# Kernel tuning notes

Hardware: AMD Instinct MI355X
Metric: run time of the kernel (lower is better)

The kernel has to match this reference:

```python
import jax, jax.numpy as jnp
import numpy as np

NUM_HEADS = 8
OUT_DIM = 32


def setup_inputs() -> dict:
    key = jax.random.key(0)
    ks = jax.random.split(key, 9)
    N, E, IN = 50000, 800000, 256
    HD = NUM_HEADS * OUT_DIM
    s = 1.0 / np.sqrt(IN)
    return {
        "h": jax.random.normal(ks[0], (N, IN), jnp.float32),
        "Wq": jax.random.normal(ks[1], (HD, IN), jnp.float32) * s,
        "bq": jax.random.normal(ks[2], (HD,), jnp.float32) * 0.01,
        "Wk": jax.random.normal(ks[3], (HD, IN), jnp.float32) * s,
        "bk": jax.random.normal(ks[4], (HD,), jnp.float32) * 0.01,
        "Wv": jax.random.normal(ks[5], (HD, IN), jnp.float32) * s,
        "bv": jax.random.normal(ks[6], (HD,), jnp.float32) * 0.01,
        "src": jax.random.randint(ks[7], (E,), 0, N, jnp.int32),
        "dst": jax.random.randint(ks[8], (E,), 0, N, jnp.int32),
    }


def reference(h, Wq, bq, Wk, bk, Wv, bv, src, dst):
    N = h.shape[0]
    H, D = NUM_HEADS, OUT_DIM
    # node projections -> [N, H, D]
    Q = (h @ Wq.T + bq).reshape(N, H, D)
    K = (h @ Wk.T + bk).reshape(N, H, D)
    V = (h @ Wv.T + bv).reshape(N, H, D)
    scale = jnp.asarray(np.sqrt(D), h.dtype)
    # per-edge scores: dot(K[src], Q[dst]) over D -> [E, H]
    score = jnp.exp(jnp.clip((K[src] * Q[dst]).sum(-1) / scale, -5.0, 5.0))
    # segment-softmax denominator over destination nodes -> [N, H]
    z = jax.ops.segment_sum(score, dst, num_segments=N)
    alpha = score / z[dst]  # [E, H]; every edge's dst has z > 0
    # weighted aggregation: sum over in-edges of alpha * V[src] -> [N, H, D]
    wV = jax.ops.segment_sum(V[src] * alpha[:, :, None], dst, num_segments=N)
    return wV
```

## Files before the change

kernel.cpp:

```cpp
#include <hip/hip_runtime.h>
#include <hip/hip_bf16.h>


typedef __attribute__((ext_vector_type(8))) short short8;
typedef __attribute__((ext_vector_type(8))) unsigned short ushortx8;
typedef __attribute__((ext_vector_type(4))) unsigned short ushortx4;
typedef __attribute__((ext_vector_type(4))) float floatx4;
typedef __attribute__((ext_vector_type(4))) int intx4;

__device__ __forceinline__ void g2l16(const void* g, void* l) {
    __builtin_amdgcn_global_load_lds(
        (const __attribute__((address_space(1))) unsigned int*)g,
        (__attribute__((address_space(3))) unsigned int*)l, 16, 0, 0);
}

__device__ __forceinline__ float bf2f(unsigned short u) {
    union { unsigned int i; float f; } c; c.i = ((unsigned int)u) << 16; return c.f;
}
__device__ __forceinline__ unsigned short f2bf(float f) {
    __hip_bfloat16 b = __float2bfloat16(f);
    return *reinterpret_cast<unsigned short*>(&b);
}

__device__ __forceinline__ ushortx4 cvt4(floatx4 f) {
    ushortx4 u;
    u.x = f2bf(f.x); u.y = f2bf(f.y); u.z = f2bf(f.z); u.w = f2bf(f.w);
    return u;
}

#define PREP_BH 1563
#define PREP_BW 16
#define PREP_BD 256

__global__ __launch_bounds__(256) void prep(
    const float* __restrict__ h, unsigned short* __restrict__ hb,
    const float* __restrict__ Wq, const float* __restrict__ Wk, const float* __restrict__ Wv,
    unsigned short* __restrict__ Wb,
    const int* __restrict__ dst, int* __restrict__ deg,
    int n4h, int n4w, int E)
{
    const int bid = blockIdx.x;
    const int tid = threadIdx.x;
    if (bid < PREP_BH) {
        const int stride = PREP_BH * 256;
        const floatx4* hs = (const floatx4*)h;
        ushortx4* hd = (ushortx4*)hb;
        int i = bid * 256 + tid;
        for (; i + 3 * stride < n4h; i += 4 * stride) {
            floatx4 f0 = __builtin_nontemporal_load(hs + i);
            floatx4 f1 = __builtin_nontemporal_load(hs + i + stride);
            floatx4 f2 = __builtin_nontemporal_load(hs + i + 2 * stride);
            floatx4 f3 = __builtin_nontemporal_load(hs + i + 3 * stride);
            hd[i] = cvt4(f0);
            hd[i + stride] = cvt4(f1);
            hd[i + 2 * stride] = cvt4(f2);
            hd[i + 3 * stride] = cvt4(f3);
        }
        for (; i < n4h; i += stride) {
            floatx4 f = __builtin_nontemporal_load(hs + i);
            hd[i] = cvt4(f);
        }
    } else if (bid < PREP_BH + 3 * PREP_BW) {
        int b2 = bid - PREP_BH;
        int mat = b2 / PREP_BW;
        const floatx4* ws = (const floatx4*)((mat == 0) ? Wq : (mat == 1) ? Wk : Wv);
        ushortx4* wd = (ushortx4*)(Wb + (size_t)mat * 65536);
        const int stride = PREP_BW * 256;
        int i = (b2 % PREP_BW) * 256 + tid;
        for (; i + 3 * stride < n4w; i += 4 * stride) {
            floatx4 f0 = __builtin_nontemporal_load(ws + i);
            floatx4 f1 = __builtin_nontemporal_load(ws + i + stride);
            floatx4 f2 = __builtin_nontemporal_load(ws + i + 2 * stride);
            floatx4 f3 = __builtin_nontemporal_load(ws + i + 3 * stride);
            wd[i] = cvt4(f0);
            wd[i + stride] = cvt4(f1);
            wd[i + 2 * stride] = cvt4(f2);
            wd[i + 3 * stride] = cvt4(f3);
        }
        for (; i < n4w; i += stride) {
            floatx4 f = __builtin_nontemporal_load(ws + i);
            wd[i] = cvt4(f);
        }
    } else {
        int b3 = bid - PREP_BH - 3 * PREP_BW;
        const int stride = PREP_BD * 256;
        const int ne4 = E >> 2;
        const intx4* ds = (const intx4*)dst;
        int i = b3 * 256 + tid;
        for (; i + stride < ne4; i += 2 * stride) {
            intx4 d0 = __builtin_nontemporal_load(ds + i);
            intx4 d1 = __builtin_nontemporal_load(ds + i + stride);
            atomicAdd(&deg[d0.x], 1); atomicAdd(&deg[d0.y], 1);
            atomicAdd(&deg[d0.z], 1); atomicAdd(&deg[d0.w], 1);
            atomicAdd(&deg[d1.x], 1); atomicAdd(&deg[d1.y], 1);
            atomicAdd(&deg[d1.z], 1); atomicAdd(&deg[d1.w], 1);
        }
        for (; i < ne4; i += stride) {
            intx4 d = __builtin_nontemporal_load(ds + i);
            atomicAdd(&deg[d.x], 1); atomicAdd(&deg[d.y], 1);
            atomicAdd(&deg[d.z], 1); atomicAdd(&deg[d.w], 1);
        }
        if (b3 == 0 && tid == 0) {
            for (int e = ne4 * 4; e < E; e++) atomicAdd(&deg[dst[e]], 1);
        }
    }
}

__global__ __launch_bounds__(256) void qkv_gemm_mfma(
    const unsigned short* __restrict__ hb, const unsigned short* __restrict__ Wb,
    const float* __restrict__ bq, const float* __restrict__ bk, const float* __restrict__ bv,
    unsigned short* __restrict__ Qb, unsigned short* __restrict__ KV, int N)
{
    __shared__ unsigned short Ast[2][128 * 32];
    __shared__ unsigned short Bst[2][128 * 32];

    const int tid = threadIdx.x;
    const int wave = tid >> 6;
    const int lane = tid & 63;
    const int m = lane & 15;
    const int q = lane >> 4;
    const int wr = wave >> 1, wc = wave & 1;

    const int nwg = gridDim.x;
    const int orig = blockIdx.x;
    const int q8 = nwg >> 3, r8 = nwg & 7;
    const int xcd = orig & 7;
    const int wgid = (xcd < r8 ? xcd * (q8 + 1) : r8 * (q8 + 1) + (xcd - r8) * q8)
                     + (orig >> 3);
    const int bx = wgid / 6;
    const int by = wgid % 6;

    const int mbase = bx * 128;
    const int mat = by >> 1;
    const int colbase = (by & 1) * 128;
    const int wrow0 = by * 128;

    const float* bias = (mat == 0) ? bq : (mat == 1) ? bk : bv;

    floatx4 acc[4][4] = {};

    for (int kk = 0; kk < 256; kk += 64) {
#pragma unroll
        for (int c = 0; c < 2; c++) {
#pragma unroll
            for (int t = 0; t < 2; t++) {
                int f = t * 256 + tid;
                int row = f >> 2, kc = f & 3;
                int grow = mbase + row; if (grow > N - 1) grow = N - 1;
                g2l16(hb + (size_t)grow * 256 + kk + c * 32 + kc * 8,
                      Ast[c] + (size_t)(t * 256 + wave * 64) * 8);
            }
#pragma unroll
            for (int t = 0; t < 2; t++) {
                int f = t * 256 + tid;
                int row = f >> 2, kc = f & 3;
                g2l16(Wb + (size_t)(wrow0 + row) * 256 + kk + c * 32 + kc * 8,
                      Bst[c] + (size_t)(t * 256 + wave * 64) * 8);
            }
        }
        __syncthreads();

#pragma unroll
        for (int c = 0; c < 2; c++) {
            short8 a[4], b[4];
#pragma unroll
            for (int i = 0; i < 4; i++) {
                int r = wr * 64 + i * 16 + m;
                a[i] = *(const short8*)&Ast[c][r * 32 + q * 8];
            }
#pragma unroll
            for (int j = 0; j < 4; j++) {
                int cc = wc * 64 + j * 16 + m;
                b[j] = *(const short8*)&Bst[c][cc * 32 + q * 8];
            }
#pragma unroll
            for (int i = 0; i < 4; i++)
#pragma unroll
                for (int j = 0; j < 4; j++)
                    acc[i][j] = __builtin_amdgcn_mfma_f32_16x16x32_bf16(a[i], b[j], acc[i][j], 0, 0, 0);
        }
        __syncthreads();
    }

    float bvj[4];
#pragma unroll
    for (int j = 0; j < 4; j++) bvj[j] = bias[colbase + wc * 64 + j * 16 + m];

    const int col0 = colbase + wc * 64 + m;
#pragma unroll
    for (int i = 0; i < 4; i++) {
#pragma unroll
        for (int r = 0; r < 4; r++) {
            int grow = mbase + wr * 64 + i * 16 + q * 4 + r;
            if (grow < N) {
                if (mat == 0) {
                    unsigned short* op = Qb + (size_t)grow * 256 + col0;
#pragma unroll
                    for (int j = 0; j < 4; j++)
                        __builtin_nontemporal_store(f2bf(acc[i][j][r] + bvj[j]), op + j * 16);
                } else {
                    unsigned short* op = KV + (size_t)grow * 512 + ((mat == 2) ? 256 : 0) + col0;
#pragma unroll
                    for (int j = 0; j < 4; j++)
                        op[j * 16] = f2bf(acc[i][j][r] + bvj[j]);
                }
            }
        }
    }
}

#define SCAN_CHUNK 2048

__global__ void scan_phase1(const int* __restrict__ deg, int* __restrict__ partials, int N) {
    __shared__ int sdata[256];
    int base = blockIdx.x * SCAN_CHUNK;
    int sum = 0;
#pragma unroll
    for (int i = 0; i < 8; i++) {
        int idx = base + threadIdx.x + i * 256;
        if (idx < N) sum += deg[idx];
    }
    sdata[threadIdx.x] = sum;
    __syncthreads();
    for (int s = 128; s > 0; s >>= 1) {
        if (threadIdx.x < (unsigned)s) sdata[threadIdx.x] += sdata[threadIdx.x + s];
        __syncthreads();
    }
    if (threadIdx.x == 0) partials[blockIdx.x] = sdata[0];
}

__global__ void scan_phase2(int* __restrict__ partials, int nb) {
    if (threadIdx.x == 0 && blockIdx.x == 0) {
        int run = 0;
        for (int i = 0; i < nb; i++) { int v = partials[i]; partials[i] = run; run += v; }
    }
}

__global__ void scan_phase3(const int* __restrict__ deg, const int* __restrict__ partials,
                            int* __restrict__ offsets, int* __restrict__ cursor, int N, int E) {
    __shared__ int sdata[256];
    int base = blockIdx.x * SCAN_CHUNK;
    int vals[8];
    int sum = 0;
#pragma unroll
    for (int i = 0; i < 8; i++) {
        int idx = base + threadIdx.x * 8 + i;
        vals[i] = (idx < N) ? deg[idx] : 0;
        sum += vals[i];
    }
    sdata[threadIdx.x] = sum;
    __syncthreads();
    for (int s = 1; s < 256; s <<= 1) {
        int v = sdata[threadIdx.x];
        int add = (threadIdx.x >= (unsigned)s) ? sdata[threadIdx.x - s] : 0;
        __syncthreads();
        sdata[threadIdx.x] = v + add;
        __syncthreads();
    }
    int excl = (threadIdx.x == 0) ? 0 : sdata[threadIdx.x - 1];
    int run = partials[blockIdx.x] + excl;
#pragma unroll
    for (int i = 0; i < 8; i++) {
        int idx = base + threadIdx.x * 8 + i;
        if (idx < N) { offsets[idx] = run; cursor[idx] = run; }
        run += vals[i];
    }
    if (blockIdx.x == 0 && threadIdx.x == 0) offsets[N] = E;
}

__global__ void scatter_edges(const int* __restrict__ dst, const int* __restrict__ src,
                              int* __restrict__ cursor, unsigned short* __restrict__ ssorted,
                              int E) {
    int e4 = (blockIdx.x * 256 + threadIdx.x) * 4;
    if (e4 + 3 < E) {
        intx4 d = __builtin_nontemporal_load((const intx4*)(dst + e4));
        intx4 s = __builtin_nontemporal_load((const intx4*)(src + e4));
        ssorted[atomicAdd(&cursor[d.x], 1)] = (unsigned short)s.x;
        ssorted[atomicAdd(&cursor[d.y], 1)] = (unsigned short)s.y;
        ssorted[atomicAdd(&cursor[d.z], 1)] = (unsigned short)s.z;
        ssorted[atomicAdd(&cursor[d.w], 1)] = (unsigned short)s.w;
    } else {
        for (int e = e4; e < E; e++)
            ssorted[atomicAdd(&cursor[dst[e]], 1)] = (unsigned short)src[e];
    }
}

__global__ __launch_bounds__(256) void edge_agg(
    const unsigned short* __restrict__ Qb, const unsigned short* __restrict__ KV,
    const int* __restrict__ offsets, const unsigned short* __restrict__ ssorted,
    float* __restrict__ out, int N)
{
    const int wave = threadIdx.x >> 6;
    const int lane = threadIdx.x & 63;
    const int half = lane >> 5;
    const int hl = lane & 31;
    const int n = blockIdx.x * 4 + wave;
    if (n >= N) return;

    float q[8];
    {
        ushortx8 qu = __builtin_nontemporal_load((const ushortx8*)(Qb + (size_t)n * 256 + hl * 8));
#pragma unroll
        for (int j = 0; j < 8; j++) q[j] = bf2f(qu[j]);
    }

    float acc[8] = {};
    float z = 0.f;
    const int beg = offsets[n], end = offsets[n + 1];
    const int len = end - beg;
    const int mid = beg + ((len + 1) >> 1);
    const float scale = 0.17677669529663687f;

    int i = half ? mid : beg;
    const int i1 = half ? end : mid;

    for (; i + 1 < i1; i += 2) {
        int s0 = __builtin_nontemporal_load(ssorted + i);
        int s1 = __builtin_nontemporal_load(ssorted + i + 1);
        const unsigned short* p0 = KV + (size_t)s0 * 512 + hl * 8;
        const unsigned short* p1 = KV + (size_t)s1 * 512 + hl * 8;
        ushortx8 k0 = *(const ushortx8*)p0;        ushortx8 v0 = *(const ushortx8*)(p0 + 256);
        ushortx8 k1 = *(const ushortx8*)p1;        ushortx8 v1 = *(const ushortx8*)(p1 + 256);

        float d0 = 0.f, d1 = 0.f;
#pragma unroll
        for (int j = 0; j < 8; j++) {
            d0 = fmaf(bf2f(k0[j]), q[j], d0);
            d1 = fmaf(bf2f(k1[j]), q[j], d1);
        }
        d0 += __shfl_xor(d0, 1); d0 += __shfl_xor(d0, 2);
        d1 += __shfl_xor(d1, 1); d1 += __shfl_xor(d1, 2);
        float e0 = __expf(fminf(5.f, fmaxf(-5.f, d0 * scale)));
        float e1 = __expf(fminf(5.f, fmaxf(-5.f, d1 * scale)));
        z += e0 + e1;
#pragma unroll
        for (int j = 0; j < 8; j++) {
            acc[j] = fmaf(e0, bf2f(v0[j]), acc[j]);
            acc[j] = fmaf(e1, bf2f(v1[j]), acc[j]);
        }
    }
    for (; i < i1; i++) {
        int s = __builtin_nontemporal_load(ssorted + i);
        const unsigned short* p = KV + (size_t)s * 512 + hl * 8;
        ushortx8 k8 = *(const ushortx8*)p;
        ushortx8 v8 = *(const ushortx8*)(p + 256);
        float d = 0.f;
#pragma unroll
        for (int j = 0; j < 8; j++) d = fmaf(bf2f(k8[j]), q[j], d);
        d += __shfl_xor(d, 1); d += __shfl_xor(d, 2);
        float sc = __expf(fminf(5.f, fmaxf(-5.f, d * scale)));
        z += sc;
#pragma unroll
        for (int j = 0; j < 8; j++) acc[j] = fmaf(sc, bf2f(v8[j]), acc[j]);
    }

    z += __shfl_xor(z, 32);
#pragma unroll
    for (int j = 0; j < 8; j++) acc[j] += __shfl_xor(acc[j], 32);

    if (half == 0) {
        float inv = (z > 0.f) ? 1.f / z : 0.f;
        floatx4 o0, o1;
        o0[0] = acc[0] * inv; o0[1] = acc[1] * inv; o0[2] = acc[2] * inv; o0[3] = acc[3] * inv;
        o1[0] = acc[4] * inv; o1[1] = acc[5] * inv; o1[2] = acc[6] * inv; o1[3] = acc[7] * inv;
        floatx4* op = (floatx4*)(out + (size_t)n * 256 + hl * 8);
        __builtin_nontemporal_store(o0, op);
        __builtin_nontemporal_store(o1, op + 1);
    }
}

extern "C" void kernel_launch(void* const* d_in, const int* in_sizes, int n_in,
                              void* d_out, int out_size, void* d_ws, size_t ws_size,
                              hipStream_t stream) {
    const float* h  = (const float*)d_in[0];
    const float* Wq = (const float*)d_in[1];
    const float* bq = (const float*)d_in[2];
    const float* Wk = (const float*)d_in[3];
    const float* bk = (const float*)d_in[4];
    const float* Wv = (const float*)d_in[5];
    const float* bv = (const float*)d_in[6];
    const int*   src = (const int*)d_in[7];
    const int*   dst = (const int*)d_in[8];
    float* out = (float*)d_out;

    const int N = in_sizes[0] / 256;
    const int E = in_sizes[7];

    size_t off = 0;
    auto alloc = [&](size_t bytes) {
        void* p = (char*)d_ws + off;
        off += (bytes + 255) & ~(size_t)255;
        return p;
    };
    unsigned short* Qb = (unsigned short*)alloc((size_t)N * 256 * 2);
    unsigned short* KV = (unsigned short*)alloc((size_t)N * 512 * 2);
    unsigned short* hb = (unsigned short*)alloc((size_t)N * 256 * 2);
    unsigned short* Wb = (unsigned short*)alloc((size_t)768 * 256 * 2);
    int* deg      = (int*)alloc((size_t)N * 4);
    int* offsets  = (int*)alloc((size_t)(N + 1) * 4);
    int* cursor   = (int*)alloc((size_t)N * 4);
    int* partials = (int*)alloc(1024 * 4);
    unsigned short* ssorted = (unsigned short*)alloc((size_t)E * 2);

    hipMemsetAsync(deg, 0, (size_t)N * 4, stream);
    int n4h = (N * 256) / 4;
    int n4w = (256 * 256) / 4;
    prep<<<PREP_BH + 3 * PREP_BW + PREP_BD, 256, 0, stream>>>(
        h, hb, Wq, Wk, Wv, Wb, dst, deg, n4h, n4w, E);

    int nb6 = ((N + 127) / 128) * 6;
    qkv_gemm_mfma<<<nb6, 256, 0, stream>>>(hb, Wb, bq, bk, bv, Qb, KV, N);

    int nscan = (N + SCAN_CHUNK - 1) / SCAN_CHUNK;
    scan_phase1<<<nscan, 256, 0, stream>>>(deg, partials, N);
    scan_phase2<<<1, 64, 0, stream>>>(partials, nscan);
    scan_phase3<<<nscan, 256, 0, stream>>>(deg, partials, offsets, cursor, N, E);
    int bc = (E + 1023) / 1024;
    scatter_edges<<<bc, 256, 0, stream>>>(dst, src, cursor, ssorted, E);

    int ablocks = (N + 3) / 4;
    edge_agg<<<ablocks, 256, 0, stream>>>(Qb, KV, offsets, ssorted, out, N);
}
```

Before: 351.6 us.

## Fold scan block-offset pass into phase3, grid-stride scatter, split aggregation launches

Removes the single-thread scan_phase2 kernel: each scan_phase3 block now sums the preceding block partials itself with a wave shuffle reduction. The edge scatter becomes a fixed 256-block grid-stride loop that processes two int4 chunks per iteration. The h-to-bf16 conversion loop is unrolled from 4 to 8 loads. The edge aggregation kernel is split into four launches over node ranges. The scan change drops a serial launch, but the partial-sum trick assumes at most 64 scan blocks, and the extra aggregation launches add launch overhead.

```diff
diff --git a/kernel.cpp b/kernel.cpp
--- a/kernel.cpp
+++ b/kernel.cpp
@@ -46,15 +46,23 @@
         const floatx4* hs = (const floatx4*)h;
         ushortx4* hd = (ushortx4*)hb;
         int i = bid * 256 + tid;
-        for (; i + 3 * stride < n4h; i += 4 * stride) {
+        for (; i + 7 * stride < n4h; i += 8 * stride) {
             floatx4 f0 = __builtin_nontemporal_load(hs + i);
             floatx4 f1 = __builtin_nontemporal_load(hs + i + stride);
             floatx4 f2 = __builtin_nontemporal_load(hs + i + 2 * stride);
             floatx4 f3 = __builtin_nontemporal_load(hs + i + 3 * stride);
+            floatx4 f4 = __builtin_nontemporal_load(hs + i + 4 * stride);
+            floatx4 f5 = __builtin_nontemporal_load(hs + i + 5 * stride);
+            floatx4 f6 = __builtin_nontemporal_load(hs + i + 6 * stride);
+            floatx4 f7 = __builtin_nontemporal_load(hs + i + 7 * stride);
             hd[i] = cvt4(f0);
             hd[i + stride] = cvt4(f1);
             hd[i + 2 * stride] = cvt4(f2);
             hd[i + 3 * stride] = cvt4(f3);
+            hd[i + 4 * stride] = cvt4(f4);
+            hd[i + 5 * stride] = cvt4(f5);
+            hd[i + 6 * stride] = cvt4(f6);
+            hd[i + 7 * stride] = cvt4(f7);
         }
         for (; i < n4h; i += stride) {
             floatx4 f = __builtin_nontemporal_load(hs + i);
@@ -229,16 +237,18 @@
     if (threadIdx.x == 0) partials[blockIdx.x] = sdata[0];
 }
 
-__global__ void scan_phase2(int* __restrict__ partials, int nb) {
-    if (threadIdx.x == 0 && blockIdx.x == 0) {
-        int run = 0;
-        for (int i = 0; i < nb; i++) { int v = partials[i]; partials[i] = run; run += v; }
-    }
-}
-
 __global__ void scan_phase3(const int* __restrict__ deg, const int* __restrict__ partials,
-                            int* __restrict__ offsets, int* __restrict__ cursor, int N, int E) {
+                            int* __restrict__ offsets, int* __restrict__ cursor,
+                            int N, int E, int nb) {
     __shared__ int sdata[256];
+    __shared__ int sbase;
+    if (threadIdx.x < 64) {
+        int v = ((int)threadIdx.x < nb && (int)threadIdx.x < (int)blockIdx.x)
+                    ? partials[threadIdx.x] : 0;
+#pragma unroll
+        for (int s = 1; s < 64; s <<= 1) v += __shfl_xor(v, s);
+        if (threadIdx.x == 0) sbase = v;
+    }
     int base = blockIdx.x * SCAN_CHUNK;
     int vals[8];
     int sum = 0;
@@ -258,7 +268,7 @@
         __syncthreads();
     }
     int excl = (threadIdx.x == 0) ? 0 : sdata[threadIdx.x - 1];
-    int run = partials[blockIdx.x] + excl;
+    int run = sbase + excl;
 #pragma unroll
     for (int i = 0; i < 8; i++) {
         int idx = base + threadIdx.x * 8 + i;
@@ -268,19 +278,41 @@
     if (blockIdx.x == 0 && threadIdx.x == 0) offsets[N] = E;
 }
 
-__global__ void scatter_edges(const int* __restrict__ dst, const int* __restrict__ src,
-                              int* __restrict__ cursor, unsigned short* __restrict__ ssorted,
-                              int E) {
-    int e4 = (blockIdx.x * 256 + threadIdx.x) * 4;
-    if (e4 + 3 < E) {
-        intx4 d = __builtin_nontemporal_load((const intx4*)(dst + e4));
-        intx4 s = __builtin_nontemporal_load((const intx4*)(src + e4));
+#define SCAT_BLOCKS 256
+__global__ __launch_bounds__(256) void scatter_edges(
+    const int* __restrict__ dst, const int* __restrict__ src,
+    int* __restrict__ cursor, unsigned short* __restrict__ ssorted, int E)
+{
+    const int t = blockIdx.x * 256 + threadIdx.x;
+    const int nt = SCAT_BLOCKS * 256;
+    const int ne4 = E >> 2;
+    const intx4* d4 = (const intx4*)dst;
+    const intx4* s4 = (const intx4*)src;
+    int i = t;
+    for (; i + nt < ne4; i += 2 * nt) {
+        intx4 d0 = __builtin_nontemporal_load(d4 + i);
+        intx4 s0 = __builtin_nontemporal_load(s4 + i);
+        intx4 d1 = __builtin_nontemporal_load(d4 + i + nt);
+        intx4 s1 = __builtin_nontemporal_load(s4 + i + nt);
+        ssorted[atomicAdd(&cursor[d0.x], 1)] = (unsigned short)s0.x;
+        ssorted[atomicAdd(&cursor[d0.y], 1)] = (unsigned short)s0.y;
+        ssorted[atomicAdd(&cursor[d0.z], 1)] = (unsigned short)s0.z;
+        ssorted[atomicAdd(&cursor[d0.w], 1)] = (unsigned short)s0.w;
+        ssorted[atomicAdd(&cursor[d1.x], 1)] = (unsigned short)s1.x;
+        ssorted[atomicAdd(&cursor[d1.y], 1)] = (unsigned short)s1.y;
+        ssorted[atomicAdd(&cursor[d1.z], 1)] = (unsigned short)s1.z;
+        ssorted[atomicAdd(&cursor[d1.w], 1)] = (unsigned short)s1.w;
+    }
+    for (; i < ne4; i += nt) {
+        intx4 d = __builtin_nontemporal_load(d4 + i);
+        intx4 s = __builtin_nontemporal_load(s4 + i);
         ssorted[atomicAdd(&cursor[d.x], 1)] = (unsigned short)s.x;
         ssorted[atomicAdd(&cursor[d.y], 1)] = (unsigned short)s.y;
         ssorted[atomicAdd(&cursor[d.z], 1)] = (unsigned short)s.z;
         ssorted[atomicAdd(&cursor[d.w], 1)] = (unsigned short)s.w;
-    } else {
-        for (int e = e4; e < E; e++)
+    }
+    if (t == 0) {
+        for (int e = ne4 * 4; e < E; e++)
             ssorted[atomicAdd(&cursor[dst[e]], 1)] = (unsigned short)src[e];
     }
 }
@@ -288,14 +320,14 @@
 __global__ __launch_bounds__(256) void edge_agg(
     const unsigned short* __restrict__ Qb, const unsigned short* __restrict__ KV,
     const int* __restrict__ offsets, const unsigned short* __restrict__ ssorted,
-    float* __restrict__ out, int N)
+    float* __restrict__ out, int n0, int n1)
 {
     const int wave = threadIdx.x >> 6;
     const int lane = threadIdx.x & 63;
     const int half = lane >> 5;
     const int hl = lane & 31;
-    const int n = blockIdx.x * 4 + wave;
-    if (n >= N) return;
+    const int n = n0 + blockIdx.x * 4 + wave;
+    if (n >= n1) return;
 
     float q[8];
     {
@@ -413,11 +445,14 @@
 
     int nscan = (N + SCAN_CHUNK - 1) / SCAN_CHUNK;
     scan_phase1<<<nscan, 256, 0, stream>>>(deg, partials, N);
-    scan_phase2<<<1, 64, 0, stream>>>(partials, nscan);
-    scan_phase3<<<nscan, 256, 0, stream>>>(deg, partials, offsets, cursor, N, E);
-    int bc = (E + 1023) / 1024;
-    scatter_edges<<<bc, 256, 0, stream>>>(dst, src, cursor, ssorted, E);
-
-    int ablocks = (N + 3) / 4;
-    edge_agg<<<ablocks, 256, 0, stream>>>(Qb, KV, offsets, ssorted, out, N);
-}
+    scan_phase3<<<nscan, 256, 0, stream>>>(deg, partials, offsets, cursor, N, E, nscan);
+    scatter_edges<<<SCAT_BLOCKS, 256, 0, stream>>>(dst, src, cursor, ssorted, E);
+
+    int q4 = (N + 3) / 4;
+    for (int c = 0; c < 4; c++) {
+        int lo = c * q4;
+        if (lo >= N) break;
+        int cnt = (N - lo < q4) ? (N - lo) : q4;
+        edge_agg<<<(cnt + 3) / 4, 256, 0, stream>>>(Qb, KV, offsets, ssorted, out, lo, lo + cnt);
+    }
+}
```

After: 367.9 us. 4.6% more time.
